# Performance work log

Hardware: AMD Instinct MI355X
Metric: run time of the kernel (lower is better)

The kernel has to match this reference:

```python
import jax, jax.numpy as jnp
import numpy as np

B, S, CIN, WIDTH, COUT = 8, 256, 3, 64, 1
MODES, BW = 32, 3


def _dct_matrix(n):
    # orthonormal DCT-II matrix; inverse = transpose (DCT-III)
    k = np.arange(n)[:, None].astype(np.float64)
    x = np.arange(n)[None, :].astype(np.float64)
    m = np.sqrt(2.0 / n) * np.cos(np.pi * (x + 0.5) * k / n)
    m[0] *= 1.0 / np.sqrt(2.0)
    return jnp.asarray(m, dtype=jnp.float32)

DCT = _dct_matrix(S)  # [S, S]


def T_fwd(u):  # u: [B, C, H, W] -> spectral coefficients
    u = jnp.einsum('kh,bchw->bckw', DCT, u)
    return jnp.einsum('lw,bckw->bckl', DCT, u)


def T_inv(c):  # inverse transform (orthonormal => transpose)
    c = jnp.einsum('kh,bckw->bchw', DCT, c)
    return jnp.einsum('lw,bclw->bclh', DCT, c).transpose(0, 1, 3, 2)


def T_inv2(c):
    # straightforward version: apply M^T along both spatial dims
    c = jnp.einsum('kh,bckl->bchl', DCT, c)
    return jnp.einsum('lw,bchl->bchw', DCT, c)


def gelu(x):
    return jax.nn.gelu(x, approximate=False)


def pseudo_spectra(u, w, cout):
    # u: [B, Cin, S, S]; w: [Cin*BW*BW, cout, MODES*MODES]
    b = T_fwd(u)
    p = MODES + BW - 1
    bp = b[:, :, :p, :p]  # pad_slices (triL=0)
    # im2col matching torch.nn.Unfold channel-major ordering (c, ki, kj)
    patches = jnp.stack([bp[:, :, i:i + MODES, j:j + MODES]
                         for i in range(BW) for j in range(BW)], axis=2)
    bs, cin = u.shape[0], u.shape[1]
    xp = patches.reshape(bs, cin * BW * BW, MODES * MODES)
    om = jnp.einsum('bix,iox->box', xp, w).reshape(bs, cout, MODES, MODES)
    out = jnp.zeros((bs, cout, S, S), u.dtype).at[:, :, :MODES, :MODES].set(om)
    return T_inv2(out)


def conv1x1(x, w, b):
    return jnp.einsum('oi,bihw->bohw', w, x) + b[None, :, None, None]


def setup_inputs() -> dict:
    key = jax.random.key(0)
    ks = jax.random.split(key, 20)
    mm = MODES * MODES
    inp = {'x': jax.random.normal(ks[0], (B, S, S, CIN), dtype=jnp.float32)}
    # PseudoSpectra weights: scale * U[0,1), scale = 1/(in*out)
    inp['wl'] = jax.random.uniform(ks[1], (CIN * BW * BW, WIDTH - CIN, mm), dtype=jnp.float32) / (CIN * (WIDTH - CIN))
    for i in range(4):
        inp[f'wc{i}'] = jax.random.uniform(ks[2 + i], (WIDTH * BW * BW, WIDTH, mm), dtype=jnp.float32) / (WIDTH * WIDTH)
    for i in range(4):
        inp[f'pw{i}'] = jax.random.normal(ks[6 + i], (WIDTH, WIDTH), dtype=jnp.float32) * 0.05
        inp[f'pb{i}'] = jnp.zeros((WIDTH,), dtype=jnp.float32)
    inp['fc1_w'] = jax.random.normal(ks[10], (WIDTH, 128), dtype=jnp.float32) * 0.05
    inp['fc1_b'] = jnp.zeros((128,), dtype=jnp.float32)
    inp['fc2_w'] = jax.random.normal(ks[11], (128, COUT), dtype=jnp.float32) * 0.05
    inp['fc2_b'] = jnp.zeros((COUT,), dtype=jnp.float32)
    return inp


def reference(x, wl, wc0, wc1, wc2, wc3,
              pw0, pb0, pw1, pb1, pw2, pb2, pw3, pb3,
              fc1_w, fc1_b, fc2_w, fc2_b):
    h = x.transpose(0, 3, 1, 2)  # [B, CIN, S, S]
    h = jnp.concatenate([h, gelu(pseudo_spectra(h, wl, WIDTH - CIN))], axis=1)
    h = h + gelu(conv1x1(h, pw0, pb0) + pseudo_spectra(h, wc0, WIDTH))
    h = h + gelu(conv1x1(h, pw1, pb1) + pseudo_spectra(h, wc1, WIDTH))
    h = h + gelu(conv1x1(h, pw2, pb2) + pseudo_spectra(h, wc2, WIDTH))
    h = h + gelu(conv1x1(h, pw3, pb3) + pseudo_spectra(h, wc3, WIDTH))
    h = h.transpose(0, 2, 3, 1)  # [B, S, S, WIDTH]
    h = gelu(h @ fc1_w + fc1_b)
    h = h @ fc2_w + fc2_b  # [B, S, S, COUT]
    y = h.transpose(0, 3, 1, 2)
    y = T_fwd(T_inv2(y))  # T(T.inv(.)) along spatial dims, as in source
    return y.transpose(0, 2, 3, 1)
```

## Files before the change

### kernel.cpp

```cpp
#include <hip/hip_runtime.h>
#include <math.h>

#define BB 8
#define S 256
#define CIN 3
#define W64 64
#define MODES 32
#define PP 34
#define KPAD 36
#define KPB 40

typedef __attribute__((ext_vector_type(8))) short bfrag;
typedef __attribute__((ext_vector_type(16))) float f32x16;

__device__ __forceinline__ float gelu_f(float x){
    float z = fabsf(x) * 0.70710678118654752f;
    float t = 1.0f / (1.0f + 0.3275911f * z);
    float p = ((((1.061405429f * t - 1.453152027f) * t) + 1.421413741f) * t
               - 0.284496736f) * t + 0.254829592f;
    float e = __expf(-z * z);
    float erf = 1.0f - p * t * e;
    erf = copysignf(erf, x);
    return 0.5f * x * (1.0f + erf);
}

__device__ __forceinline__ void split_bf(float x, short &hi, short &lo){
    unsigned u = __float_as_uint(x);
    unsigned r = u + 0x7FFFu + ((u >> 16) & 1u);
    hi = (short)(r >> 16);
    float hf = __uint_as_float(r & 0xFFFF0000u);
    float l = x - hf;
    unsigned v = __float_as_uint(l);
    unsigned s2 = v + 0x7FFFu + ((v >> 16) & 1u);
    lo = (short)(s2 >> 16);
}

__device__ __forceinline__ void split8(float4 a, float4 b, bfrag &hv, bfrag &lv){
    short hi, lo;
    split_bf(a.x, hi, lo); hv[0] = hi; lv[0] = lo;
    split_bf(a.y, hi, lo); hv[1] = hi; lv[1] = lo;
    split_bf(a.z, hi, lo); hv[2] = hi; lv[2] = lo;
    split_bf(a.w, hi, lo); hv[3] = hi; lv[3] = lo;
    split_bf(b.x, hi, lo); hv[4] = hi; lv[4] = lo;
    split_bf(b.y, hi, lo); hv[5] = hi; lv[5] = lo;
    split_bf(b.z, hi, lo); hv[6] = hi; lv[6] = lo;
    split_bf(b.w, hi, lo); hv[7] = hi; lv[7] = lo;
}

__global__ void k_init_dt(float* __restrict__ dt, short* __restrict__ dth,
                          short* __restrict__ dtl){
    int tid = blockIdx.x * 256 + threadIdx.x;
    if (tid >= S * KPB) return;
    int h = tid / KPB, k = tid % KPB;
    double v = 0.0;
    if (k < PP) {
        v = sqrt(2.0 / (double)S) * cos(3.14159265358979323846 * (h + 0.5) * k / (double)S);
        if (k == 0) v *= 0.70710678118654752440;
    }
    float f = (float)v;
    if (k < KPAD) dt[h * KPAD + k] = f;
    short hi, lo; split_bf(f, hi, lo);
    dth[tid] = hi; dtl[tid] = lo;
}

__global__ void k_prep_pw(const float* __restrict__ pw, short* __restrict__ pwh,
                          short* __restrict__ pwl){
    int e = blockIdx.x * 256 + threadIdx.x;
    if (e >= 4096) return;
    short hi, lo; split_bf(pw[e], hi, lo);
    pwh[e] = hi; pwl[e] = lo;
}

__global__ void k_prep_fc1(const float* __restrict__ fc1w, short* __restrict__ f1h,
                           short* __restrict__ f1l){
    int e = blockIdx.x * 256 + threadIdx.x;
    if (e >= 8192) return;
    int i = e >> 7, j = e & 127;
    int n = j >> 5, ks = i >> 4;
    int l = (j & 31) + (((i & 15) >= 8) ? 32 : 0);
    int jr = i & 7;
    int idx = ((n * 4 + ks) * 64 + l) * 8 + jr;
    short hi, lo; split_bf(fc1w[e], hi, lo);
    f1h[idx] = hi; f1l[idx] = lo;
}

__global__ void k_copy_x(const float* __restrict__ x, float* __restrict__ h){
    int e = blockIdx.x * 256 + threadIdx.x;
    if (e >= BB * S * S * CIN) return;
    int px = e / CIN, c = e % CIN;
    h[(size_t)px * W64 + c] = x[e];
}

template<int C>
__global__ void k_fwd1(const float* __restrict__ src, float* __restrict__ tmp1,
                       const float* __restrict__ dt){
    int b = blockIdx.y;
    int idx = blockIdx.x * 256 + threadIdx.x;
    if (idx >= S * C) return;
    float acc[PP];
    #pragma unroll
    for (int k = 0; k < PP; k++) acc[k] = 0.f;
    const float* sp = src + (size_t)b * S * S * C + idx;
    for (int hh = 0; hh < S; hh++){
        float v = sp[(size_t)hh * S * C];
        const float* dr = dt + hh * KPAD;
        #pragma unroll
        for (int k = 0; k < PP; k++) acc[k] = fmaf(dr[k], v, acc[k]);
    }
    float* op = tmp1 + (size_t)b * PP * S * C + idx;
    #pragma unroll
    for (int k = 0; k < PP; k++) op[(size_t)k * S * C] = acc[k];
}

__global__ void k_fwd2_3(const float* __restrict__ tmp1, float* __restrict__ bp,
                         const float* __restrict__ dt){
    const int C = 3;
    int b = blockIdx.y;
    int idx = blockIdx.x * 256 + threadIdx.x;
    if (idx >= PP * C) return;
    int k = idx / C, c = idx % C;
    float acc[PP];
    #pragma unroll
    for (int l = 0; l < PP; l++) acc[l] = 0.f;
    const float* sp = tmp1 + ((size_t)b * PP + k) * S * C + c;
    for (int w = 0; w < S; w++){
        float v = sp[(size_t)w * C];
        const float* dr = dt + w * KPAD;
        #pragma unroll
        for (int l = 0; l < PP; l++) acc[l] = fmaf(dr[l], v, acc[l]);
    }
    float* op = bp + ((size_t)b * PP + k) * PP * C + c;
    #pragma unroll
    for (int l = 0; l < PP; l++) op[(size_t)l * C] = acc[l];
}

__global__ __launch_bounds__(256, 4) void k_fwd2_64(
        const float* __restrict__ tmp1, float* __restrict__ bp,
        const float* __restrict__ dt){
    const int C = 64;
    __shared__ float red[4 * PP * 66];
    int k = blockIdx.x, b = blockIdx.y;
    int t = threadIdx.x;
    int c = t & 63;
    int ws = __builtin_amdgcn_readfirstlane(t >> 6);
    float acc[PP];
    #pragma unroll
    for (int l = 0; l < PP; l++) acc[l] = 0.f;
    const float* sp = tmp1 + ((size_t)b * PP + k) * S * C + c;
    for (int w = ws * 64; w < ws * 64 + 64; w++){
        float v = sp[(size_t)w * C];
        const float* dr = dt + w * KPAD;
        #pragma unroll
        for (int l = 0; l < PP; l++) acc[l] = fmaf(dr[l], v, acc[l]);
    }
    #pragma unroll
    for (int l = 0; l < PP; l++) red[(ws * PP + l) * 66 + c] = acc[l];
    __syncthreads();
    float* op = bp + ((size_t)b * PP + k) * PP * C;
    for (int e = t; e < PP * C; e += 256){
        int l = e >> 6, cc = e & 63;
        op[e] = red[(0 * PP + l) * 66 + cc] + red[(1 * PP + l) * 66 + cc]
              + red[(2 * PP + l) * 66 + cc] + red[(3 * PP + l) * 66 + cc];
    }
}

template<int C, int CC>
__global__ void k_xp_gather(const float* __restrict__ bp, float* __restrict__ xp){
    __shared__ float lds[8 * 3 * PP * (CC + 1)];
    int k  = blockIdx.x;
    int c0 = blockIdx.y * CC;
    int t  = threadIdx.x;
    const int TOT = 8 * 3 * PP * CC;
    for (int e = t; e < TOT; e += 256){
        int b   = e / (3 * PP * CC);
        int r   = e % (3 * PP * CC);
        int row = r / (PP * CC);
        int r2  = r % (PP * CC);
        int l   = r2 / CC;
        int c   = r2 % CC;
        lds[((b * 3 + row) * PP + l) * (CC + 1) + c] =
            bp[(((size_t)b * PP + (k + row)) * PP + l) * C + c0 + c];
    }
    __syncthreads();
    int l = t >> 3;
    int b = t & 7;
    for (int c = 0; c < CC; c++){
        #pragma unroll
        for (int ij = 0; ij < 9; ij++){
            int i_ = ij / 3, j_ = ij % 3;
            int i  = (c0 + c) * 9 + ij;
            float v = lds[((b * 3 + i_) * PP + (l + j_)) * (CC + 1) + c];
            xp[((size_t)i * 1024 + k * 32 + l) * 8 + b] = v;
        }
    }
}

template<int ITOT, int O>
__global__ void k_om(const float* __restrict__ xp, const float* __restrict__ w,
                     float* __restrict__ part){
    int bx  = blockIdx.x;
    int klt = bx & 31;
    int ot  = (bx >> 5) & 7;
    int ns  = bx >> 8;
    const int ILEN = ITOT / 3;
    int t  = threadIdx.x;
    int kl = klt * 32 + (t & 31);
    int o  = ot * 8 + (t >> 5);
    if (o >= O) return;
    float a0=0,a1=0,a2=0,a3=0,a4=0,a5=0,a6=0,a7=0;
    const float* xpp = xp + ((size_t)(ns * ILEN) * 1024 + kl) * 8;
    const float* wp  = w + ((size_t)(ns * ILEN) * O + o) * 1024 + kl;
    #pragma unroll 4
    for (int i = 0; i < ILEN; i++){
        float4 xa = *(const float4*)(xpp + (size_t)i * 8192);
        float4 xb = *(const float4*)(xpp + (size_t)i * 8192 + 4);
        float wv  = wp[(size_t)i * O * 1024];
        a0 = fmaf(xa.x, wv, a0); a1 = fmaf(xa.y, wv, a1);
        a2 = fmaf(xa.z, wv, a2); a3 = fmaf(xa.w, wv, a3);
        a4 = fmaf(xb.x, wv, a4); a5 = fmaf(xb.y, wv, a5);
        a6 = fmaf(xb.z, wv, a6); a7 = fmaf(xb.w, wv, a7);
    }
    float* pp = part + (size_t)ns * 8 * 64 * 1024;
    pp[((size_t)0 * 64 + o) * 1024 + kl] = a0;
    pp[((size_t)1 * 64 + o) * 1024 + kl] = a1;
    pp[((size_t)2 * 64 + o) * 1024 + kl] = a2;
    pp[((size_t)3 * 64 + o) * 1024 + kl] = a3;
    pp[((size_t)4 * 64 + o) * 1024 + kl] = a4;
    pp[((size_t)5 * 64 + o) * 1024 + kl] = a5;
    pp[((size_t)6 * 64 + o) * 1024 + kl] = a6;
    pp[((size_t)7 * 64 + o) * 1024 + kl] = a7;
}

template<int O>
__global__ void k_inv1(const float* __restrict__ part, float* __restrict__ t2,
                       const float* __restrict__ dt){
    __shared__ float oms[32 * 65];
    const int N = 8 * 64 * 1024;
    int wc = blockIdx.x, k = blockIdx.y, b = blockIdx.z;
    int t = threadIdx.x;
    for (int e = t; e < 2048; e += 256){
        int o_ = e >> 5, l = e & 31;
        int idx = ((b * 64 + o_) << 10) + k * 32 + l;
        oms[l * 65 + o_] = part[idx] + part[N + idx] + part[2 * N + idx];
    }
    __syncthreads();
    int o  = t & 63;
    int wg = __builtin_amdgcn_readfirstlane(t >> 6);
    int wbase = wc * 32 + wg * 8;
    float acc[8];
    #pragma unroll
    for (int wj = 0; wj < 8; wj++) acc[wj] = 0.f;
    for (int l = 0; l < 32; l++){
        float ov = oms[l * 65 + o];
        #pragma unroll
        for (int wj = 0; wj < 8; wj++)
            acc[wj] = fmaf(dt[(wbase + wj) * KPAD + l], ov, acc[wj]);
    }
    if (o < O){
        #pragma unroll
        for (int wj = 0; wj < 8; wj++)
            t2[(((size_t)b * 32 + k) * S + wbase + wj) * 64 + o] = acc[wj];
    }
}

template<bool CONV>
__global__ __launch_bounds__(256, 3) void k_fused(
        const float* __restrict__ t2, float* __restrict__ h,
        const short* __restrict__ pwh, const short* __restrict__ pwl,
        const float* __restrict__ pb,
        const short* __restrict__ dth, const short* __restrict__ dtl){
    __shared__ short t2fh[8 * 64 * 8];
    __shared__ short t2fl[8 * 64 * 8];
    __shared__ short hsfh[CONV ? 8 * 64 * 8 : 1];
    __shared__ short hsfl[CONV ? 8 * 64 * 8 : 1];
    __shared__ float hres[CONV ? 64 * 64 : 1];
    int wt = blockIdx.x, b = blockIdx.y;
    int t = threadIdx.x;

    #pragma unroll
    for (int e2 = 0; e2 < 2; e2++){
        int e = t + e2 * 256;
        int le = e & 63, ks = (e >> 6) & 1, ne = e >> 7;
        int oe = (ne & 1) * 32 + (le & 31);
        int we = wt * 2 + (ne >> 1);
        int k0 = ks * 16 + (le >> 5) * 8;
        bfrag hv, lv;
        #pragma unroll
        for (int j = 0; j < 8; j++){
            short hi, lo;
            split_bf(t2[((size_t)(b * 32 + k0 + j) * S + we) * 64 + oe], hi, lo);
            hv[j] = hi; lv[j] = lo;
        }
        int idx = ((ne * 2 + ks) * 64 + le) * 8;
        *(bfrag*)(t2fh + idx) = hv;
        *(bfrag*)(t2fl + idx) = lv;
    }

    int l = t & 63;
    int n = t >> 6;
    int oh = n & 1, wl = n >> 1;
    int o = oh * 32 + (l & 31);

    int ihalf = t & 7;
    int pxA = t >> 3;
    int pxB = pxA + 32;
    const float* hb = h + ((size_t)b * S * S + (size_t)wt * 2) * 64;
    size_t offA = ((size_t)(pxA >> 1) * S + (pxA & 1)) * 64 + ihalf * 8;
    size_t offB = ((size_t)(pxB >> 1) * S + (pxB & 1)) * 64 + ihalf * 8;
    float4 a0, a1, b0, b1;
    if (CONV){
        a0 = *(const float4*)(hb + offA);
        a1 = *(const float4*)(hb + offA + 4);
        b0 = *(const float4*)(hb + offB);
        b1 = *(const float4*)(hb + offB + 4);
    }

    for (int ht = 0; ht < 8; ht++){
        if (CONV){
            int ks = ihalf >> 1;
            int lh = (ihalf & 1) * 32;
            bfrag hv, lv;
            split8(a0, a1, hv, lv);
            int idx = (((pxA & 1) * 4 + ks) * 64 + (pxA >> 1) + lh) * 8;
            *(bfrag*)(hsfh + idx) = hv;
            *(bfrag*)(hsfl + idx) = lv;
            *(float4*)(hres + pxA * 64 + ihalf * 8)     = a0;
            *(float4*)(hres + pxA * 64 + ihalf * 8 + 4) = a1;
            split8(b0, b1, hv, lv);
            idx = (((pxB & 1) * 4 + ks) * 64 + (pxB >> 1) + lh) * 8;
            *(bfrag*)(hsfh + idx) = hv;
            *(bfrag*)(hsfl + idx) = lv;
            *(float4*)(hres + pxB * 64 + ihalf * 8)     = b0;
            *(float4*)(hres + pxB * 64 + ihalf * 8 + 4) = b1;
        }
        __syncthreads();
        if (CONV && ht < 7){
            const float* hb2 = hb + (size_t)(ht + 1) * 32 * S * 64;
            a0 = *(const float4*)(hb2 + offA);
            a1 = *(const float4*)(hb2 + offA + 4);
            b0 = *(const float4*)(hb2 + offB);
            b1 = *(const float4*)(hb2 + offB + 4);
        }

        f32x16 acc = {0,0,0,0,0,0,0,0,0,0,0,0,0,0,0,0};

        int hh0 = ht * 32;
        #pragma unroll
        for (int ks = 0; ks < 2; ks++){
            int aoff = (hh0 + (l & 31)) * KPB + ks * 16 + (l >> 5) * 8;
            bfrag ah = *(const bfrag*)(dth + aoff);
            bfrag al = *(const bfrag*)(dtl + aoff);
            int boff = ((n * 2 + ks) * 64 + l) * 8;
            bfrag bh = *(const bfrag*)(t2fh + boff);
            bfrag bl = *(const bfrag*)(t2fl + boff);
            acc = __builtin_amdgcn_mfma_f32_32x32x16_bf16(ah, bh, acc, 0, 0, 0);
            acc = __builtin_amdgcn_mfma_f32_32x32x16_bf16(ah, bl, acc, 0, 0, 0);
            acc = __builtin_amdgcn_mfma_f32_32x32x16_bf16(al, bh, acc, 0, 0, 0);
        }

        if (CONV){
            #pragma unroll
            for (int ks = 0; ks < 4; ks++){
                int aoff = ((wl * 4 + ks) * 64 + l) * 8;
                bfrag ah = *(const bfrag*)(hsfh + aoff);
                bfrag al = *(const bfrag*)(hsfl + aoff);
                int boff = o * 64 + ks * 16 + (l >> 5) * 8;
                bfrag bh = *(const bfrag*)(pwh + boff);
                bfrag bl = *(const bfrag*)(pwl + boff);
                acc = __builtin_amdgcn_mfma_f32_32x32x16_bf16(ah, bh, acc, 0, 0, 0);
                acc = __builtin_amdgcn_mfma_f32_32x32x16_bf16(ah, bl, acc, 0, 0, 0);
                acc = __builtin_amdgcn_mfma_f32_32x32x16_bf16(al, bh, acc, 0, 0, 0);
            }
            float pbv = pb[o];
            #pragma unroll
            for (int r = 0; r < 16; r++){
                int row = (r & 3) + 8 * (r >> 2) + 4 * (l >> 5);
                float res = hres[(row * 2 + wl) * 64 + o];
                size_t pix = ((size_t)b * S + ht * 32 + row) * S + wt * 2 + wl;
                h[pix * 64 + o] = res + gelu_f(acc[r] + pbv);
            }
        } else {
            if (o < 61){
                #pragma unroll
                for (int r = 0; r < 16; r++){
                    int row = (r & 3) + 8 * (r >> 2) + 4 * (l >> 5);
                    size_t pix = ((size_t)b * S + ht * 32 + row) * S + wt * 2 + wl;
                    h[pix * 64 + 3 + o] = gelu_f(acc[r]);
                }
            }
        }
        __syncthreads();
    }
}

__global__ __launch_bounds__(256, 4) void k_mlp(
        const float* __restrict__ h, const short* __restrict__ f1h,
        const short* __restrict__ f1l, const float* __restrict__ fc1b,
        const float* __restrict__ fc2w, const float* __restrict__ fc2b,
        float* __restrict__ out){
    __shared__ short ah_[2 * 4 * 64 * 8];
    __shared__ short al_[2 * 4 * 64 * 8];
    __shared__ float red[2 * 64 * 33];
    size_t base = (size_t)blockIdx.x * 64;
    int t = threadIdx.x;
    const float* hrow = h + base * 64;
    #pragma unroll
    for (int e2 = 0; e2 < 2; e2++){
        int e = t + e2 * 256;
        int px = e >> 3, ih = e & 7;
        float4 v0 = *(const float4*)(hrow + px * 64 + ih * 8);
        float4 v1 = *(const float4*)(hrow + px * 64 + ih * 8 + 4);
        bfrag hv, lv;
        split8(v0, v1, hv, lv);
        int ks = ih >> 1, lh = (ih & 1) * 32, m = px >> 5;
        int idx = ((m * 4 + ks) * 64 + (px & 31) + lh) * 8;
        *(bfrag*)(ah_ + idx) = hv;
        *(bfrag*)(al_ + idx) = lv;
    }
    __syncthreads();
    int l = t & 63;
    int w = t >> 6;
    int m = w >> 1;
    int n0 = (w & 1) * 2;
    f32x16 acc0 = {0,0,0,0,0,0,0,0,0,0,0,0,0,0,0,0};
    f32x16 acc1 = {0,0,0,0,0,0,0,0,0,0,0,0,0,0,0,0};
    #pragma unroll
    for (int ks = 0; ks < 4; ks++){
        int aoff = ((m * 4 + ks) * 64 + l) * 8;
        bfrag ah = *(const bfrag*)(ah_ + aoff);
        bfrag al = *(const bfrag*)(al_ + aoff);
        int b0off = ((n0 * 4 + ks) * 64 + l) * 8;
        int b1off = (((n0 + 1) * 4 + ks) * 64 + l) * 8;
        bfrag b0h = *(const bfrag*)(f1h + b0off);
        bfrag b0l = *(const bfrag*)(f1l + b0off);
        bfrag b1h = *(const bfrag*)(f1h + b1off);
        bfrag b1l = *(const bfrag*)(f1l + b1off);
        acc0 = __builtin_amdgcn_mfma_f32_32x32x16_bf16(ah, b0h, acc0, 0, 0, 0);
        acc0 = __builtin_amdgcn_mfma_f32_32x32x16_bf16(ah, b0l, acc0, 0, 0, 0);
        acc0 = __builtin_amdgcn_mfma_f32_32x32x16_bf16(al, b0h, acc0, 0, 0, 0);
        acc1 = __builtin_amdgcn_mfma_f32_32x32x16_bf16(ah, b1h, acc1, 0, 0, 0);
        acc1 = __builtin_amdgcn_mfma_f32_32x32x16_bf16(ah, b1l, acc1, 0, 0, 0);
        acc1 = __builtin_amdgcn_mfma_f32_32x32x16_bf16(al, b1h, acc1, 0, 0, 0);
    }
    int j0 = n0 * 32 + (l & 31), j1 = j0 + 32;
    float b10 = fc1b[j0], b11 = fc1b[j1];
    float f20 = fc2w[j0], f21 = fc2w[j1];
    float* rb = red + (w & 1) * 64 * 33;
    #pragma unroll
    for (int r = 0; r < 16; r++){
        int row = (r & 3) + 8 * (r >> 2) + 4 * (l >> 5);
        rb[(m * 32 + row) * 33 + (l & 31)] =
            gelu_f(acc0[r] + b10) * f20 + gelu_f(acc1[r] + b11) * f21;
    }
    __syncthreads();
    if (t < 64){
        float s = fc2b[0];
        #pragma unroll
        for (int c = 0; c < 32; c++)
            s += red[t * 33 + c] + red[(64 + t) * 33 + c];
        out[base + t] = s;
    }
}

extern "C" void kernel_launch(void* const* d_in, const int* in_sizes, int n_in,
                              void* d_out, int out_size, void* d_ws, size_t ws_size,
                              hipStream_t stream) {
    const float* x    = (const float*)d_in[0];
    const float* wl   = (const float*)d_in[1];
    const float* wc[4] = {(const float*)d_in[2], (const float*)d_in[3],
                          (const float*)d_in[4], (const float*)d_in[5]};
    const float* pw[4] = {(const float*)d_in[6], (const float*)d_in[8],
                          (const float*)d_in[10], (const float*)d_in[12]};
    const float* pb[4] = {(const float*)d_in[7], (const float*)d_in[9],
                          (const float*)d_in[11], (const float*)d_in[13]};
    const float* fc1w = (const float*)d_in[14];
    const float* fc1b = (const float*)d_in[15];
    const float* fc2w = (const float*)d_in[16];
    const float* fc2b = (const float*)d_in[17];
    float* out = (float*)d_out;

    char* ws = (char*)d_ws;
    size_t off = 0;
    float* dt   = (float*)(ws + off); off += (size_t)S * KPAD * 4;
    short* dth  = (short*)(ws + off); off += (size_t)S * KPB * 2;
    short* dtl  = (short*)(ws + off); off += (size_t)S * KPB * 2;
    short* pwh  = (short*)(ws + off); off += (size_t)4 * 4096 * 2;
    short* pwl  = (short*)(ws + off); off += (size_t)4 * 4096 * 2;
    short* f1h  = (short*)(ws + off); off += (size_t)8192 * 2;
    short* f1l  = (short*)(ws + off); off += (size_t)8192 * 2;
    float* h    = (float*)(ws + off); off += (size_t)BB * S * S * W64 * 4;
    float* tmp1 = (float*)(ws + off); off += (size_t)BB * PP * S * W64 * 4;
    float* bp   = (float*)(ws + off); off += (size_t)BB * PP * PP * W64 * 4;
    float* xp   = (float*)(ws + off); off += (size_t)576 * 1024 * 8 * 4;
    float* part = (float*)(ws + off); off += (size_t)3 * 8 * 64 * 1024 * 4;
    float* t2   = (float*)(ws + off); off += (size_t)BB * 32 * S * W64 * 4;

    k_init_dt<<<(S * KPB + 255) / 256, 256, 0, stream>>>(dt, dth, dtl);
    for (int i = 0; i < 4; i++)
        k_prep_pw<<<16, 256, 0, stream>>>(pw[i], pwh + i * 4096, pwl + i * 4096);
    k_prep_fc1<<<32, 256, 0, stream>>>(fc1w, f1h, f1l);
    k_copy_x<<<(BB * S * S * CIN + 255) / 256, 256, 0, stream>>>(x, h);

    k_fwd1<3><<<dim3(3, BB), 256, 0, stream>>>(x, tmp1, dt);
    k_fwd2_3<<<dim3(1, BB), 256, 0, stream>>>(tmp1, bp, dt);
    k_xp_gather<3, 3><<<dim3(32, 1), 256, 0, stream>>>(bp, xp);
    k_om<27, 61><<<768, 256, 0, stream>>>(xp, wl, part);
    k_inv1<61><<<dim3(8, 32, BB), 256, 0, stream>>>(part, t2, dt);
    k_fused<false><<<dim3(128, BB), 256, 0, stream>>>(
        t2, h, nullptr, nullptr, nullptr, dth, dtl);

    for (int blk = 0; blk < 4; blk++){
        k_fwd1<64><<<dim3(64, BB), 256, 0, stream>>>(h, tmp1, dt);
        k_fwd2_64<<<dim3(PP, BB), 256, 0, stream>>>(tmp1, bp, dt);
        k_xp_gather<64, 16><<<dim3(32, 4), 256, 0, stream>>>(bp, xp);
        k_om<576, 64><<<768, 256, 0, stream>>>(xp, wc[blk], part);
        k_inv1<64><<<dim3(8, 32, BB), 256, 0, stream>>>(part, t2, dt);
        k_fused<true><<<dim3(128, BB), 256, 0, stream>>>(
            t2, h, pwh + blk * 4096, pwl + blk * 4096, pb[blk], dth, dtl);
    }

    k_mlp<<<dim3(BB * S * S / 64), 256, 0, stream>>>(h, f1h, f1l, fc1b, fc2w, fc2b, out);
}
```

Before: 1.268 ms.

## Drop LDS residual buffer, XOR-swizzle fragment layout, raise fused kernel occupancy

Removes the 16KB hres shared buffer from the fused conv kernel and re-reads the residual directly from global h just before writing it back. The launch-bounds occupancy hint rises from 3 to 5 blocks per SM now that LDS usage is smaller. It also applies an XOR swizzle (row ^ group) to the bf16 fragment layout in LDS in both the fused and MLP kernels to reduce bank conflicts on the stores. The cost is an extra global read per output element and possible register pressure from the tighter launch bound.

```diff
diff --git a/kernel.cpp b/kernel.cpp
--- a/kernel.cpp
+++ b/kernel.cpp
@@ -264,7 +264,7 @@
 }
 
 template<bool CONV>
-__global__ __launch_bounds__(256, 3) void k_fused(
+__global__ __launch_bounds__(256, 5) void k_fused(
         const float* __restrict__ t2, float* __restrict__ h,
         const short* __restrict__ pwh, const short* __restrict__ pwl,
         const float* __restrict__ pb,
@@ -273,7 +273,6 @@
     __shared__ short t2fl[8 * 64 * 8];
     __shared__ short hsfh[CONV ? 8 * 64 * 8 : 1];
     __shared__ short hsfl[CONV ? 8 * 64 * 8 : 1];
-    __shared__ float hres[CONV ? 64 * 64 : 1];
     int wt = blockIdx.x, b = blockIdx.y;
     int t = threadIdx.x;
 
@@ -319,19 +318,16 @@
         if (CONV){
             int ks = ihalf >> 1;
             int lh = (ihalf & 1) * 32;
+            int g  = (pxA & 1) * 4 + ks;
             bfrag hv, lv;
             split8(a0, a1, hv, lv);
-            int idx = (((pxA & 1) * 4 + ks) * 64 + (pxA >> 1) + lh) * 8;
-            *(bfrag*)(hsfh + idx) = hv;
-            *(bfrag*)(hsfl + idx) = lv;
-            *(float4*)(hres + pxA * 64 + ihalf * 8)     = a0;
-            *(float4*)(hres + pxA * 64 + ihalf * 8 + 4) = a1;
+            int rowA = (pxA >> 1) + lh;
+            *(bfrag*)(hsfh + (g * 64 + (rowA ^ g)) * 8) = hv;
+            *(bfrag*)(hsfl + (g * 64 + (rowA ^ g)) * 8) = lv;
             split8(b0, b1, hv, lv);
-            idx = (((pxB & 1) * 4 + ks) * 64 + (pxB >> 1) + lh) * 8;
-            *(bfrag*)(hsfh + idx) = hv;
-            *(bfrag*)(hsfl + idx) = lv;
-            *(float4*)(hres + pxB * 64 + ihalf * 8)     = b0;
-            *(float4*)(hres + pxB * 64 + ihalf * 8 + 4) = b1;
+            int rowB = (pxB >> 1) + lh;
+            *(bfrag*)(hsfh + (g * 64 + (rowB ^ g)) * 8) = hv;
+            *(bfrag*)(hsfl + (g * 64 + (rowB ^ g)) * 8) = lv;
         }
         __syncthreads();
         if (CONV && ht < 7){
@@ -361,7 +357,8 @@
         if (CONV){
             #pragma unroll
             for (int ks = 0; ks < 4; ks++){
-                int aoff = ((wl * 4 + ks) * 64 + l) * 8;
+                int g = wl * 4 + ks;
+                int aoff = (g * 64 + (l ^ g)) * 8;
                 bfrag ah = *(const bfrag*)(hsfh + aoff);
                 bfrag al = *(const bfrag*)(hsfl + aoff);
                 int boff = o * 64 + ks * 16 + (l >> 5) * 8;
@@ -375,8 +372,8 @@
             #pragma unroll
             for (int r = 0; r < 16; r++){
                 int row = (r & 3) + 8 * (r >> 2) + 4 * (l >> 5);
-                float res = hres[(row * 2 + wl) * 64 + o];
                 size_t pix = ((size_t)b * S + ht * 32 + row) * S + wt * 2 + wl;
+                float res = h[pix * 64 + o];
                 h[pix * 64 + o] = res + gelu_f(acc[r] + pbv);
             }
         } else {
@@ -412,10 +409,10 @@
         float4 v1 = *(const float4*)(hrow + px * 64 + ih * 8 + 4);
         bfrag hv, lv;
         split8(v0, v1, hv, lv);
-        int ks = ih >> 1, lh = (ih & 1) * 32, m = px >> 5;
-        int idx = ((m * 4 + ks) * 64 + (px & 31) + lh) * 8;
-        *(bfrag*)(ah_ + idx) = hv;
-        *(bfrag*)(al_ + idx) = lv;
+        int g = (px >> 5) * 4 + (ih >> 1);
+        int row = (px & 31) + (ih & 1) * 32;
+        *(bfrag*)(ah_ + (g * 64 + (row ^ g)) * 8) = hv;
+        *(bfrag*)(al_ + (g * 64 + (row ^ g)) * 8) = lv;
     }
     __syncthreads();
     int l = t & 63;
@@ -426,7 +423,8 @@
     f32x16 acc1 = {0,0,0,0,0,0,0,0,0,0,0,0,0,0,0,0};
     #pragma unroll
     for (int ks = 0; ks < 4; ks++){
-        int aoff = ((m * 4 + ks) * 64 + l) * 8;
+        int g = m * 4 + ks;
+        int aoff = (g * 64 + (l ^ g)) * 8;
         bfrag ah = *(const bfrag*)(ah_ + aoff);
         bfrag al = *(const bfrag*)(al_ + aoff);
         int b0off = ((n0 * 4 + ks) * 64 + l) * 8;
```

Result: slower. 1.322 ms (+4.3%).
